# Performance work log

Measured on AMD Instinct MI355X. Metric: run time of the kernel, lower is better.

The kernel has to match this reference:

```python
import jax, jax.numpy as jnp
import numpy as np

THETA_BINS = 8
PHI_BINS = 8
BLOCK_SIZE = 15  # odd, per assert
STRIDE = 1       # with stride=1, nr_block along each axis == image dim
EPS = 2.220446049250313e-16  # sys.float_info.epsilon, as in the original


def setup_inputs() -> dict:
    key = jax.random.key(0)
    x = jax.random.normal(key, (96, 96, 96), dtype=jnp.float32)
    return {"x": x}


def _sliding_sum0(a, bs):
    """Sliding-window sum of size bs along axis 0, stride 1, nblocks = a.shape[0].
    Windows extending past the end see zeros (original code indexes past the image;
    we treat out-of-range voxels as zero contribution)."""
    pad = [(0, bs - 1)] + [(0, 0)] * (a.ndim - 1)
    cs = jnp.cumsum(jnp.pad(a, pad), axis=0)
    cs = jnp.concatenate([jnp.zeros_like(cs[:1]), cs], axis=0)  # exclusive prefix
    return cs[bs:] - cs[:-bs]  # out[i] = sum a[i:i+bs]


def reference(x):
    Z, Y, X = x.shape
    Tb, Pb, BS = THETA_BINS, PHI_BINS, BLOCK_SIZE
    B = Tb * Pb

    # conv3d with fixed central-difference kernels, padding=1 (zero pad)
    p = jnp.pad(x, 1)
    gz = p[2:, 1:-1, 1:-1] - p[:-2, 1:-1, 1:-1]
    gy = p[1:-1, 2:, 1:-1] - p[1:-1, :-2, 1:-1]
    gx = p[1:-1, 1:-1, 2:] - p[1:-1, 1:-1, :-2]

    r = jnp.sqrt(gx * gx + gy * gy + gz * gz)
    theta = jnp.arctan(gy / (gx + EPS))          # range (-pi/2, pi/2)
    phi = jnp.arccos(gz / (r + EPS))             # range [0, pi]

    two_pi = jnp.float32(2.0 * np.pi)
    theta = jnp.where(theta < 0, theta + two_pi, theta)  # angle_normalizer(theta,0,2pi)

    t_raw = theta / (two_pi / Tb)
    p_raw = phi / (jnp.float32(np.pi) / Pb)

    lt = jnp.floor(t_raw).astype(jnp.int32)
    lt = jnp.where(lt == Tb, 0, lt)
    lp = jnp.floor(p_raw).astype(jnp.int32)
    lp = jnp.where(lp == Pb, 0, lp)
    ht = (lt + 1) % Tb
    hp = (lp + 1) % Pb

    # NOTE: the original uses the THETA fractional part for the phi ratios too
    # (a bug in the source) - reproduced faithfully here.
    frac = t_raw - jnp.floor(t_raw)
    w_lo = jnp.minimum(frac, 1.0 - frac)   # low-bin ratio per the branchy original
    w_hi = 1.0 - w_lo                      # high-bin ratio
    wp_lo = jnp.where(frac == 0, jnp.float32(1.0), w_lo)  # frac==0 -> phi not split
    wp_hi = 1.0 - wp_lo

    # per-voxel soft-binned histogram volume [N, B] via 4 scatter-adds
    n = r.size
    rows = jnp.arange(n)
    rf = r.reshape(-1)
    ltf, htf = lt.reshape(-1), ht.reshape(-1)
    lpf, hpf = lp.reshape(-1), hp.reshape(-1)
    wlof, whif = w_lo.reshape(-1), w_hi.reshape(-1)
    wplof, wphif = wp_lo.reshape(-1), wp_hi.reshape(-1)

    V = jnp.zeros((n, B), dtype=r.dtype)
    V = V.at[rows, ltf * Pb + lpf].add(rf * wlof * wplof)
    V = V.at[rows, htf * Pb + lpf].add(rf * whif * wplof)
    V = V.at[rows, ltf * Pb + hpf].add(rf * wlof * wphif)
    V = V.at[rows, htf * Pb + hpf].add(rf * whif * wphif)
    V = V.reshape(Z, Y, X, B)

    # block histograms: separable sliding-window sum over block_size^3, stride 1
    for ax in (0, 1, 2):
        V = jnp.moveaxis(_sliding_sum0(jnp.moveaxis(V, ax, 0), BS), 0, ax)

    return V[None, None]  # [1, 1, nbz, nby, nbx, theta_bins*phi_bins]
```

## Files before the change

kernel.cpp:

```cpp
#include <hip/hip_runtime.h>

typedef _Float16 half_t;
typedef __attribute__((ext_vector_type(8))) _Float16 half8;
typedef __attribute__((ext_vector_type(4))) _Float16 half4;

#define DIM 96
#define NBINS 64
#define BSZ 15
#define PADROWS (DIM + BSZ - 1)
#define NTHREADS 256
#define RS_F 68
#define RS4_F 17
#define RS_H 72

__device__ __forceinline__ void bin_line_to_lds(
    const float* __restrict__ in, float* __restrict__ V,
    const int y, const int z, const int tid)
{
    if (tid < DIM) {
        const int x = tid;
        const int idx = (z * DIM + y) * DIM + x;
        const float xm = (x > 0)       ? in[idx - 1]         : 0.0f;
        const float xp = (x < DIM - 1) ? in[idx + 1]         : 0.0f;
        const float ym = (y > 0)       ? in[idx - DIM]       : 0.0f;
        const float yp = (y < DIM - 1) ? in[idx + DIM]       : 0.0f;
        const float zm = (z > 0)       ? in[idx - DIM * DIM] : 0.0f;
        const float zp = (z < DIM - 1) ? in[idx + DIM * DIM] : 0.0f;
        const float gx = xp - xm, gy = yp - ym, gz = zp - zm;

        const float EPSF  = 2.220446049250313e-16f;
        const float TWOPI = 6.28318530717958647692f;
        const float PIF   = 3.14159265358979323846f;

        const float r = sqrtf(gx * gx + gy * gy + gz * gz);
        float theta = atanf(gy / (gx + EPSF));
        const float phi = acosf(gz / (r + EPSF));
        if (theta < 0.0f) theta += TWOPI;
        const float t_raw = theta / (TWOPI / 8.0f);
        const float p_raw = phi   / (PIF   / 8.0f);
        const float ft = floorf(t_raw);
        const float fp = floorf(p_raw);
        int lt = (int)ft; if (lt == 8) lt = 0;
        int lp = (int)fp; if (lp == 8) lp = 0;
        const int ht = (lt + 1) & 7;
        const int hp = (lp + 1) & 7;
        const float frac  = t_raw - ft;
        const float w_lo  = fminf(frac, 1.0f - frac);
        const float w_hi  = 1.0f - w_lo;
        const float wp_lo = (frac == 0.0f) ? 1.0f : w_lo;
        const float wp_hi = 1.0f - wp_lo;

        float* vrow = V + x * RS_F;
        vrow[lt * 8 + lp] += r * w_lo * wp_lo;
        vrow[ht * 8 + lp] += r * w_hi * wp_lo;
        vrow[lt * 8 + hp] += r * w_lo * wp_hi;
        vrow[ht * 8 + hp] += r * w_hi * wp_hi;
    }
}

__global__ __launch_bounds__(NTHREADS) void k1_bin_xsum_h(
    const float* __restrict__ in, half_t* __restrict__ ws1)
{
    __shared__ float V[PADROWS * RS_F];
    const int tid = threadIdx.x;
    const int y = blockIdx.x, z = blockIdx.y;

    for (int i = tid; i < PADROWS * RS4_F; i += NTHREADS)
        ((float4*)V)[i] = make_float4(0.f, 0.f, 0.f, 0.f);
    __syncthreads();
    bin_line_to_lds(in, V, y, z, tid);
    __syncthreads();

    const int c8 = tid & 7;
    const int strip = tid >> 3;
    int pos = strip * 3;
    const float4* V4 = (const float4*)V;

    float acc[8];
    #pragma unroll
    for (int k = 0; k < 8; ++k) acc[k] = 0.f;
    #pragma unroll
    for (int d = 0; d < BSZ; ++d) {
        const float4 a = V4[(pos + d) * RS4_F + c8 * 2];
        const float4 b = V4[(pos + d) * RS4_F + c8 * 2 + 1];
        acc[0] += a.x; acc[1] += a.y; acc[2] += a.z; acc[3] += a.w;
        acc[4] += b.x; acc[5] += b.y; acc[6] += b.z; acc[7] += b.w;
    }
    #pragma unroll
    for (int j = 0; j < 3; ++j) {
        half8 o;
        #pragma unroll
        for (int k = 0; k < 8; ++k) o[k] = (half_t)acc[k];
        *(half8*)(ws1 + (((size_t)(z * DIM + y) * DIM + pos) * NBINS + c8 * 8)) = o;
        if (j < 2) {
            const float4 a0 = V4[pos * RS4_F + c8 * 2];
            const float4 b0 = V4[pos * RS4_F + c8 * 2 + 1];
            const float4 a1 = V4[(pos + BSZ) * RS4_F + c8 * 2];
            const float4 b1 = V4[(pos + BSZ) * RS4_F + c8 * 2 + 1];
            acc[0] += a1.x - a0.x; acc[1] += a1.y - a0.y;
            acc[2] += a1.z - a0.z; acc[3] += a1.w - a0.w;
            acc[4] += b1.x - b0.x; acc[5] += b1.y - b0.y;
            acc[6] += b1.z - b0.z; acc[7] += b1.w - b0.w;
            ++pos;
        }
    }
}

__global__ __launch_bounds__(NTHREADS) void k2_ysum_h(
    const half_t* __restrict__ ws1, half_t* __restrict__ ws2)
{
    __shared__ half_t H[PADROWS * RS_H];
    const int tid = threadIdx.x;
    const int x = blockIdx.x, z = blockIdx.y;

    for (int i = tid; i < DIM * 8; i += NTHREADS) {
        const int pos = i >> 3, c8 = i & 7;
        *(half8*)&H[pos * RS_H + c8 * 8] =
            *(const half8*)(ws1 + (((size_t)(z * DIM + pos) * DIM + x) * NBINS + c8 * 8));
    }
    for (int i = tid; i < (PADROWS - DIM) * 8; i += NTHREADS) {
        const int pos = DIM + (i >> 3), c8 = i & 7;
        half8 zv = {};
        *(half8*)&H[pos * RS_H + c8 * 8] = zv;
    }
    __syncthreads();

    const int c8 = tid & 7;
    const int strip = tid >> 3;
    int pos = strip * 3;

    float acc[8];
    #pragma unroll
    for (int k = 0; k < 8; ++k) acc[k] = 0.f;
    #pragma unroll
    for (int d = 0; d < BSZ; ++d) {
        const half8 hv = *(const half8*)&H[(pos + d) * RS_H + c8 * 8];
        #pragma unroll
        for (int k = 0; k < 8; ++k) acc[k] += (float)hv[k];
    }
    #pragma unroll
    for (int j = 0; j < 3; ++j) {
        half8 o;
        #pragma unroll
        for (int k = 0; k < 8; ++k) o[k] = (half_t)acc[k];
        *(half8*)(ws2 + (((size_t)(z * DIM + pos) * DIM + x) * NBINS + c8 * 8)) = o;
        if (j < 2) {
            const half8 hs = *(const half8*)&H[pos * RS_H + c8 * 8];
            const half8 ha = *(const half8*)&H[(pos + BSZ) * RS_H + c8 * 8];
            #pragma unroll
            for (int k = 0; k < 8; ++k) acc[k] += (float)ha[k] - (float)hs[k];
            ++pos;
        }
    }
}

__global__ __launch_bounds__(NTHREADS) void k3_zsum_h(
    const half_t* __restrict__ ws2, float* __restrict__ out)
{
    __shared__ half_t H[PADROWS * RS_H];
    const int tid = threadIdx.x;
    const int x = blockIdx.x, y = blockIdx.y;

    for (int i = tid; i < DIM * 8; i += NTHREADS) {
        const int pos = i >> 3, c8 = i & 7;
        *(half8*)&H[pos * RS_H + c8 * 8] =
            *(const half8*)(ws2 + (((size_t)(pos * DIM + y) * DIM + x) * NBINS + c8 * 8));
    }
    for (int i = tid; i < (PADROWS - DIM) * 8; i += NTHREADS) {
        const int pos = DIM + (i >> 3), c8 = i & 7;
        half8 zv = {};
        *(half8*)&H[pos * RS_H + c8 * 8] = zv;
    }
    __syncthreads();

    const int c4 = tid & 15;
    const int strip = tid >> 4;
    int pos = strip * 6;

    float4 s = make_float4(0.f, 0.f, 0.f, 0.f);
    #pragma unroll
    for (int d = 0; d < BSZ; ++d) {
        const half4 hv = *(const half4*)&H[(pos + d) * RS_H + c4 * 4];
        s.x += (float)hv[0]; s.y += (float)hv[1];
        s.z += (float)hv[2]; s.w += (float)hv[3];
    }
    float4* out4 = (float4*)out;
    #pragma unroll
    for (int j = 0; j < 6; ++j) {
        out4[((size_t)(pos * DIM + y) * DIM + x) * 16 + c4] = s;
        if (j < 5) {
            const half4 hs = *(const half4*)&H[pos * RS_H + c4 * 4];
            const half4 ha = *(const half4*)&H[(pos + BSZ) * RS_H + c4 * 4];
            s.x += (float)ha[0] - (float)hs[0]; s.y += (float)ha[1] - (float)hs[1];
            s.z += (float)ha[2] - (float)hs[2]; s.w += (float)ha[3] - (float)hs[3];
            ++pos;
        }
    }
}

__global__ __launch_bounds__(NTHREADS) void k1_bin_xsum_f(
    const float* __restrict__ in, float* __restrict__ out)
{
    __shared__ float V[PADROWS * RS_F];
    const int tid = threadIdx.x;
    const int y = blockIdx.x, z = blockIdx.y;

    for (int i = tid; i < PADROWS * RS4_F; i += NTHREADS)
        ((float4*)V)[i] = make_float4(0.f, 0.f, 0.f, 0.f);
    __syncthreads();
    bin_line_to_lds(in, V, y, z, tid);
    __syncthreads();

    const int c4 = tid & 15;
    const int strip = tid >> 4;
    int pos = strip * 6;
    const float4* V4 = (const float4*)V;

    float4 s = make_float4(0.f, 0.f, 0.f, 0.f);
    #pragma unroll
    for (int d = 0; d < BSZ; ++d) {
        const float4 v = V4[(pos + d) * RS4_F + c4];
        s.x += v.x; s.y += v.y; s.z += v.z; s.w += v.w;
    }
    float4* out4 = (float4*)out;
    const int base = (z * DIM + y) * DIM * 16;
    out4[base + pos * 16 + c4] = s;
    #pragma unroll
    for (int j = 1; j < 6; ++j) {
        const float4 a = V4[pos * RS4_F + c4];
        const float4 b = V4[(pos + BSZ) * RS4_F + c4];
        s.x += b.x - a.x; s.y += b.y - a.y; s.z += b.z - a.z; s.w += b.w - a.w;
        ++pos;
        out4[base + pos * 16 + c4] = s;
    }
}

__global__ __launch_bounds__(NTHREADS) void k_axis_sum_f(
    float* __restrict__ data, const int mulY, const int stride4)
{
    __shared__ float4 V4[PADROWS * RS4_F];
    const int tid = threadIdx.x;
    const int base4 = (blockIdx.y * mulY + blockIdx.x) * 16;
    float4* data4 = (float4*)data;

    for (int i = tid; i < DIM * 16; i += NTHREADS) {
        const int pos = i >> 4, c4 = i & 15;
        V4[pos * RS4_F + c4] = data4[base4 + (size_t)pos * stride4 + c4];
    }
    for (int i = tid; i < (PADROWS - DIM) * 16; i += NTHREADS) {
        const int pos = DIM + (i >> 4), c4 = i & 15;
        V4[pos * RS4_F + c4] = make_float4(0.f, 0.f, 0.f, 0.f);
    }
    __syncthreads();

    const int c4 = tid & 15;
    const int strip = tid >> 4;
    int pos = strip * 6;

    float4 s = make_float4(0.f, 0.f, 0.f, 0.f);
    #pragma unroll
    for (int d = 0; d < BSZ; ++d) {
        const float4 v = V4[(pos + d) * RS4_F + c4];
        s.x += v.x; s.y += v.y; s.z += v.z; s.w += v.w;
    }
    data4[base4 + (size_t)pos * stride4 + c4] = s;
    #pragma unroll
    for (int j = 1; j < 6; ++j) {
        const float4 a = V4[pos * RS4_F + c4];
        const float4 b = V4[(pos + BSZ) * RS4_F + c4];
        s.x += b.x - a.x; s.y += b.y - a.y; s.z += b.z - a.z; s.w += b.w - a.w;
        ++pos;
        data4[base4 + (size_t)pos * stride4 + c4] = s;
    }
}

extern "C" void kernel_launch(void* const* d_in, const int* in_sizes, int n_in,
                              void* d_out, int out_size, void* d_ws, size_t ws_size,
                              hipStream_t stream) {
    (void)in_sizes; (void)n_in; (void)out_size;
    const float* x = (const float*)d_in[0];
    float* out = (float*)d_out;
    const size_t nvox = (size_t)DIM * DIM * DIM * NBINS;
    const size_t need = 2 * nvox * sizeof(half_t);

    dim3 grid(DIM, DIM), block(NTHREADS);
    if (ws_size >= need) {
        half_t* ws1 = (half_t*)d_ws;
        half_t* ws2 = ws1 + nvox;
        k1_bin_xsum_h<<<grid, block, 0, stream>>>(x, ws1);
        k2_ysum_h<<<grid, block, 0, stream>>>(ws1, ws2);
        k3_zsum_h<<<grid, block, 0, stream>>>(ws2, out);
    } else {
        k1_bin_xsum_f<<<grid, block, 0, stream>>>(x, out);
        k_axis_sum_f<<<grid, block, 0, stream>>>(out, DIM * DIM * 16, DIM * 16);
        k_axis_sum_f<<<grid, block, 0, stream>>>(out, DIM * 16, DIM * DIM * 16);
    }
}
```

Before: 335.5 us.

## Fuse y-axis sliding sum into binning kernel via running LDS window

Replaces the separate binning/x-sum and y-sum kernels with one kernel that handles a tile of 4 y rows per block. It keeps a running y-window of per-voxel histograms in LDS, adding the incoming line and subtracting the outgoing one, so the x-sum output is already y-summed. This removes one full fp16 workspace round trip through global memory and one kernel launch. In exchange each block recomputes the gradient binning for 14 extra lines (roughly 4.5x redundant binning work), and float add/subtract in the running window can accumulate cancellation error.

```diff
diff --git a/kernel.cpp b/kernel.cpp
--- a/kernel.cpp
+++ b/kernel.cpp
@@ -12,10 +12,12 @@
 #define RS_F 68
 #define RS4_F 17
 #define RS_H 72
-
-__device__ __forceinline__ void bin_line_to_lds(
+#define TY 4
+#define YTILES (DIM / TY)
+
+__device__ __forceinline__ void bin_line_scatter(
     const float* __restrict__ in, float* __restrict__ V,
-    const int y, const int z, const int tid)
+    const int y, const int z, const int tid, const float sgn)
 {
     if (tid < DIM) {
         const int x = tid;
@@ -50,107 +52,75 @@
         const float wp_lo = (frac == 0.0f) ? 1.0f : w_lo;
         const float wp_hi = 1.0f - wp_lo;
 
+        const float rs = r * sgn;
         float* vrow = V + x * RS_F;
-        vrow[lt * 8 + lp] += r * w_lo * wp_lo;
-        vrow[ht * 8 + lp] += r * w_hi * wp_lo;
-        vrow[lt * 8 + hp] += r * w_lo * wp_hi;
-        vrow[ht * 8 + hp] += r * w_hi * wp_hi;
-    }
-}
-
-__global__ __launch_bounds__(NTHREADS) void k1_bin_xsum_h(
+        vrow[lt * 8 + lp] += rs * w_lo * wp_lo;
+        vrow[ht * 8 + lp] += rs * w_hi * wp_lo;
+        vrow[lt * 8 + hp] += rs * w_lo * wp_hi;
+        vrow[ht * 8 + hp] += rs * w_hi * wp_hi;
+    }
+}
+
+__global__ __launch_bounds__(NTHREADS) void kA_bin_xy_h(
     const float* __restrict__ in, half_t* __restrict__ ws1)
 {
     __shared__ float V[PADROWS * RS_F];
     const int tid = threadIdx.x;
-    const int y = blockIdx.x, z = blockIdx.y;
+    const int y0 = blockIdx.x * TY;
+    const int z  = blockIdx.y;
 
     for (int i = tid; i < PADROWS * RS4_F; i += NTHREADS)
         ((float4*)V)[i] = make_float4(0.f, 0.f, 0.f, 0.f);
     __syncthreads();
-    bin_line_to_lds(in, V, y, z, tid);
-    __syncthreads();
+
+    #pragma unroll
+    for (int j = 0; j < BSZ - 1; ++j) {
+        const int ys = y0 + j;
+        if (ys < DIM) bin_line_scatter(in, V, ys, z, tid, 1.0f);
+    }
 
     const int c8 = tid & 7;
     const int strip = tid >> 3;
-    int pos = strip * 3;
+    const int pos0 = strip * 3;
     const float4* V4 = (const float4*)V;
 
-    float acc[8];
-    #pragma unroll
-    for (int k = 0; k < 8; ++k) acc[k] = 0.f;
-    #pragma unroll
-    for (int d = 0; d < BSZ; ++d) {
-        const float4 a = V4[(pos + d) * RS4_F + c8 * 2];
-        const float4 b = V4[(pos + d) * RS4_F + c8 * 2 + 1];
-        acc[0] += a.x; acc[1] += a.y; acc[2] += a.z; acc[3] += a.w;
-        acc[4] += b.x; acc[5] += b.y; acc[6] += b.z; acc[7] += b.w;
-    }
-    #pragma unroll
-    for (int j = 0; j < 3; ++j) {
-        half8 o;
+    for (int r = 0; r < TY; ++r) {
+        const int y = y0 + r;
+        if (y + BSZ - 1 < DIM) bin_line_scatter(in, V, y + BSZ - 1, z, tid, 1.0f);
+        __syncthreads();
+
+        float acc[8];
         #pragma unroll
-        for (int k = 0; k < 8; ++k) o[k] = (half_t)acc[k];
-        *(half8*)(ws1 + (((size_t)(z * DIM + y) * DIM + pos) * NBINS + c8 * 8)) = o;
-        if (j < 2) {
-            const float4 a0 = V4[pos * RS4_F + c8 * 2];
-            const float4 b0 = V4[pos * RS4_F + c8 * 2 + 1];
-            const float4 a1 = V4[(pos + BSZ) * RS4_F + c8 * 2];
-            const float4 b1 = V4[(pos + BSZ) * RS4_F + c8 * 2 + 1];
-            acc[0] += a1.x - a0.x; acc[1] += a1.y - a0.y;
-            acc[2] += a1.z - a0.z; acc[3] += a1.w - a0.w;
-            acc[4] += b1.x - b0.x; acc[5] += b1.y - b0.y;
-            acc[6] += b1.z - b0.z; acc[7] += b1.w - b0.w;
-            ++pos;
+        for (int k = 0; k < 8; ++k) acc[k] = 0.f;
+        #pragma unroll
+        for (int d = 0; d < BSZ; ++d) {
+            const float4 a = V4[(pos0 + d) * RS4_F + c8 * 2];
+            const float4 b = V4[(pos0 + d) * RS4_F + c8 * 2 + 1];
+            acc[0] += a.x; acc[1] += a.y; acc[2] += a.z; acc[3] += a.w;
+            acc[4] += b.x; acc[5] += b.y; acc[6] += b.z; acc[7] += b.w;
         }
-    }
-}
-
-__global__ __launch_bounds__(NTHREADS) void k2_ysum_h(
-    const half_t* __restrict__ ws1, half_t* __restrict__ ws2)
-{
-    __shared__ half_t H[PADROWS * RS_H];
-    const int tid = threadIdx.x;
-    const int x = blockIdx.x, z = blockIdx.y;
-
-    for (int i = tid; i < DIM * 8; i += NTHREADS) {
-        const int pos = i >> 3, c8 = i & 7;
-        *(half8*)&H[pos * RS_H + c8 * 8] =
-            *(const half8*)(ws1 + (((size_t)(z * DIM + pos) * DIM + x) * NBINS + c8 * 8));
-    }
-    for (int i = tid; i < (PADROWS - DIM) * 8; i += NTHREADS) {
-        const int pos = DIM + (i >> 3), c8 = i & 7;
-        half8 zv = {};
-        *(half8*)&H[pos * RS_H + c8 * 8] = zv;
-    }
-    __syncthreads();
-
-    const int c8 = tid & 7;
-    const int strip = tid >> 3;
-    int pos = strip * 3;
-
-    float acc[8];
-    #pragma unroll
-    for (int k = 0; k < 8; ++k) acc[k] = 0.f;
-    #pragma unroll
-    for (int d = 0; d < BSZ; ++d) {
-        const half8 hv = *(const half8*)&H[(pos + d) * RS_H + c8 * 8];
+        int pos = pos0;
         #pragma unroll
-        for (int k = 0; k < 8; ++k) acc[k] += (float)hv[k];
-    }
-    #pragma unroll
-    for (int j = 0; j < 3; ++j) {
-        half8 o;
-        #pragma unroll
-        for (int k = 0; k < 8; ++k) o[k] = (half_t)acc[k];
-        *(half8*)(ws2 + (((size_t)(z * DIM + pos) * DIM + x) * NBINS + c8 * 8)) = o;
-        if (j < 2) {
-            const half8 hs = *(const half8*)&H[pos * RS_H + c8 * 8];
-            const half8 ha = *(const half8*)&H[(pos + BSZ) * RS_H + c8 * 8];
+        for (int j = 0; j < 3; ++j) {
+            half8 o;
             #pragma unroll
-            for (int k = 0; k < 8; ++k) acc[k] += (float)ha[k] - (float)hs[k];
-            ++pos;
+            for (int k = 0; k < 8; ++k) o[k] = (half_t)acc[k];
+            *(half8*)(ws1 + (((size_t)(z * DIM + y) * DIM + pos) * NBINS + c8 * 8)) = o;
+            if (j < 2) {
+                const float4 a0 = V4[pos * RS4_F + c8 * 2];
+                const float4 b0 = V4[pos * RS4_F + c8 * 2 + 1];
+                const float4 a1 = V4[(pos + BSZ) * RS4_F + c8 * 2];
+                const float4 b1 = V4[(pos + BSZ) * RS4_F + c8 * 2 + 1];
+                acc[0] += a1.x - a0.x; acc[1] += a1.y - a0.y;
+                acc[2] += a1.z - a0.z; acc[3] += a1.w - a0.w;
+                acc[4] += b1.x - b0.x; acc[5] += b1.y - b0.y;
+                acc[6] += b1.z - b0.z; acc[7] += b1.w - b0.w;
+                ++pos;
+            }
         }
+        __syncthreads();
+        if (r < TY - 1)
+            bin_line_scatter(in, V, y, z, tid, -1.0f);
     }
 }
 
@@ -208,7 +178,7 @@
     for (int i = tid; i < PADROWS * RS4_F; i += NTHREADS)
         ((float4*)V)[i] = make_float4(0.f, 0.f, 0.f, 0.f);
     __syncthreads();
-    bin_line_to_lds(in, V, y, z, tid);
+    bin_line_scatter(in, V, y, z, tid, 1.0f);
     __syncthreads();
 
     const int c4 = tid & 15;
@@ -281,18 +251,16 @@
     const float* x = (const float*)d_in[0];
     float* out = (float*)d_out;
     const size_t nvox = (size_t)DIM * DIM * DIM * NBINS;
-    const size_t need = 2 * nvox * sizeof(half_t);
-
-    dim3 grid(DIM, DIM), block(NTHREADS);
+    const size_t need = nvox * sizeof(half_t);
+
+    dim3 block(NTHREADS);
     if (ws_size >= need) {
         half_t* ws1 = (half_t*)d_ws;
-        half_t* ws2 = ws1 + nvox;
-        k1_bin_xsum_h<<<grid, block, 0, stream>>>(x, ws1);
-        k2_ysum_h<<<grid, block, 0, stream>>>(ws1, ws2);
-        k3_zsum_h<<<grid, block, 0, stream>>>(ws2, out);
+        kA_bin_xy_h<<<dim3(YTILES, DIM), block, 0, stream>>>(x, ws1);
+        k3_zsum_h<<<dim3(DIM, DIM), block, 0, stream>>>(ws1, out);
     } else {
-        k1_bin_xsum_f<<<grid, block, 0, stream>>>(x, out);
-        k_axis_sum_f<<<grid, block, 0, stream>>>(out, DIM * DIM * 16, DIM * 16);
-        k_axis_sum_f<<<grid, block, 0, stream>>>(out, DIM * 16, DIM * DIM * 16);
-    }
-}
+        k1_bin_xsum_f<<<dim3(DIM, DIM), block, 0, stream>>>(x, out);
+        k_axis_sum_f<<<dim3(DIM, DIM), block, 0, stream>>>(out, DIM * DIM * 16, DIM * 16);
+        k_axis_sum_f<<<dim3(DIM, DIM), block, 0, stream>>>(out, DIM * 16, DIM * DIM * 16);
+    }
+}
```

Result: faster. 326.9 us (-2.6%).
